# Optimization experiments

Hardware: AMD Instinct MI355X
Metric: run time of the kernel (lower is better)

## Reference

```python
import jax, jax.numpy as jnp
import numpy as np

H = 8192   # lattice vertex count (all levels, synthetic, == hash_cnt)
N0 = 8192  # output point count
F = 15     # permutohedral filter size: (t+1)^(d+1) - t^(d+1), t=1, d=3
NEG = 0.1  # LeakyReLU negative slope

def lrelu(x):
    return jnp.where(x >= 0, x, NEG * x)

def conv1x1(x, w, b):
    # x (B,C,N), w (O,C), b (O,)
    return jnp.einsum('oc,bcn->bon', w, x) + b[None, :, None]

def splat(feat, bary, offset, num):
    # barycentric scatter of point features onto lattice: (B,C,N)->(B,C,num)
    w = feat[:, :, None, :] * bary[:, None, :, :]  # (B,C,4,N)
    def one(wb, ob):
        C = wb.shape[0]
        return jax.ops.segment_sum(wb.reshape(C, -1).T, ob.reshape(-1), num_segments=num).T
    return jax.vmap(one)(w, offset)

def gather(lat, idx):
    # lat (B,C,H), idx (B,K,N) -> (B,C,K,N)
    return jax.vmap(lambda f, i: f[:, i])(lat, idx)

def slice_lat(lat, bary, offset):
    # barycentric interpolation from lattice back to points: (B,C,N)
    return jnp.einsum('bcjn,bjn->bcn', gather(lat, offset), bary)

def blur_mlp(lat, nbrs, w0, b0, w1, b1):
    # BilateralConvFlex blur: gather F lattice neighbors, 1x1-conv MLP (last_relu=False)
    g = gather(lat, nbrs)  # (B,C,F,H)
    B, C, Fk, Hk = g.shape
    h = lrelu(conv1x1(g.reshape(B, C * Fk, Hk), w0, b0))
    return conv1x1(h, w1, b1)

def corr_block(feat1_pts, feat2_lat, prev_pts, bary1, off1, out_bary, out_off,
               idx1, idx2, wc0, bc0, wc1, bc1, wo0, bo0, wo1, bo1):
    # BilateralCorrelationFlex: splat pc1, hash-indexed patch correlation with pc2
    # lattice, per-displacement corr MLP, flatten over displacements, out MLP, slice.
    L1 = splat(feat1_pts, bary1, off1, H)                  # (B,C,H)
    x = gather(L1, idx1) * gather(feat2_lat, idx2)         # (B,C,F,H)
    if prev_pts is not None:
        P1 = splat(prev_pts, bary1, off1, H)
        x = jnp.concatenate([x, gather(P1, idx1)], axis=1)
    h = lrelu(jnp.einsum('oc,bcfh->bofh', wc0, x) + bc0[None, :, None, None])
    h = lrelu(jnp.einsum('oc,bcfh->bofh', wc1, h) + bc1[None, :, None, None])
    B, Co, Fk, Hk = h.shape
    h = lrelu(conv1x1(h.reshape(B, Co * Fk, Hk), wo0, bo0))
    h = conv1x1(h, wo1, bo1)                               # last_relu=False
    return slice_lat(h, out_bary, out_off)

def setup_inputs():
    key = jax.random.key(0)
    ks = iter(jax.random.split(key, 100))
    def randn(shape):
        return jax.random.normal(next(ks), shape, dtype=jnp.float32)
    def bary(n):
        b = jax.random.uniform(next(ks), (1, 4, n), dtype=jnp.float32)
        return b / jnp.sum(b, axis=1, keepdims=True)
    def ridx(shape, hi):
        return jax.random.randint(next(ks), shape, 0, hi)
    def W(o, c):
        return jax.random.normal(next(ks), (o, c), dtype=jnp.float32) / np.float32(np.sqrt(c))
    def bias(o):
        return jax.random.normal(next(ks), (o,), dtype=jnp.float32) * 0.01
    inp = {}
    for n in ['feat0_1', 'feat0_2', 'feat0_4', 'feat1_1', 'feat1_2', 'feat1_4']:
        inp[n] = randn((1, 32, H))
    for n in ['g2_pc1_el_minus_gr', 'g2_pc2_el_minus_gr', 'g1_pc1_el_minus_gr', 'g1_pc2_el_minus_gr']:
        inp[n] = randn((1, 4, H))
    inp['g2_pc1_barycentric'] = bary(H); inp['g2_pc2_barycentric'] = bary(H)
    inp['g1_pc1_barycentric'] = bary(H); inp['g1_pc2_barycentric'] = bary(H)
    inp['g0_pc1_barycentric'] = bary(N0)
    for n in ['g2_pc1_lattice_offset', 'g2_pc2_lattice_offset', 'g1_pc1_lattice_offset', 'g1_pc2_lattice_offset']:
        inp[n] = ridx((1, 4, H), H)
    inp['g0_pc1_lattice_offset'] = ridx((1, 4, N0), H)
    for n in ['g1_pc1_blur_neighbors', 'g1_pc2_blur_neighbors', 'g0_pc1_blur_neighbors', 'g0_pc2_blur_neighbors',
              'g1_pc1_corr_indices', 'g1_pc2_corr_indices', 'g0_pc1_corr_indices', 'g0_pc2_corr_indices']:
        inp[n] = ridx((1, F, H), H)
    inp['w_embed2'] = W(128, 32); inp['b_embed2'] = bias(128)
    inp['w_embed1'] = W(256, 32); inp['b_embed1'] = bias(256)
    inp['w_up2_0'] = W(256, 132 * F); inp['b_up2_0'] = bias(256)
    inp['w_up2_1'] = W(256, 256); inp['b_up2_1'] = bias(256)
    inp['w_up1_0'] = W(512, 516 * F); inp['b_up1_0'] = bias(512)
    inp['w_up1_1'] = W(512, 512); inp['b_up1_1'] = bias(512)
    inp['w_c2_corr0'] = W(32, 256); inp['b_c2_corr0'] = bias(32)
    inp['w_c2_corr1'] = W(32, 32); inp['b_c2_corr1'] = bias(32)
    inp['w_c2_out0'] = W(256, 32 * F); inp['b_c2_out0'] = bias(256)
    inp['w_c2_out1'] = W(256, 256); inp['b_c2_out1'] = bias(256)
    inp['w_c1_corr0'] = W(32, 512 + 256); inp['b_c1_corr0'] = bias(32)
    inp['w_c1_corr1'] = W(32, 32); inp['b_c1_corr1'] = bias(32)
    inp['w_c1_out0'] = W(512, 32 * F); inp['b_c1_out0'] = bias(512)
    inp['w_c1_out1'] = W(512, 512); inp['b_c1_out1'] = bias(512)
    inp['w_s4'] = W(512, 512); inp['b_s4'] = bias(512)
    inp['w_s2'] = W(256, 512); inp['b_s2'] = bias(256)
    inp['w_s1'] = W(3, 256); inp['b_s1'] = bias(3)
    return inp

def reference(feat0_1, feat0_2, feat0_4, feat1_1, feat1_2, feat1_4,
              g2_pc1_el_minus_gr, g2_pc2_el_minus_gr, g1_pc1_el_minus_gr, g1_pc2_el_minus_gr,
              g2_pc1_barycentric, g2_pc2_barycentric, g1_pc1_barycentric, g1_pc2_barycentric, g0_pc1_barycentric,
              g2_pc1_lattice_offset, g2_pc2_lattice_offset, g1_pc1_lattice_offset, g1_pc2_lattice_offset, g0_pc1_lattice_offset,
              g1_pc1_blur_neighbors, g1_pc2_blur_neighbors, g0_pc1_blur_neighbors, g0_pc2_blur_neighbors,
              g1_pc1_corr_indices, g1_pc2_corr_indices, g0_pc1_corr_indices, g0_pc2_corr_indices,
              w_embed2, b_embed2, w_embed1, b_embed1,
              w_up2_0, b_up2_0, w_up2_1, b_up2_1, w_up1_0, b_up1_0, w_up1_1, b_up1_1,
              w_c2_corr0, b_c2_corr0, w_c2_corr1, b_c2_corr1, w_c2_out0, b_c2_out0, w_c2_out1, b_c2_out1,
              w_c1_corr0, b_c1_corr0, w_c1_corr1, b_c1_corr1, w_c1_out0, b_c1_out0, w_c1_out1, b_c1_out1,
              w_s4, b_s4, w_s2, b_s2, w_s1, b_s1):
    # conv4_embed and feat*_4 are defined but unused in the original forward.
    f0_2 = lrelu(conv1x1(feat0_2, w_embed2, b_embed2))
    f1_2 = lrelu(conv1x1(feat1_2, w_embed2, b_embed2))
    blur0 = blur_mlp(jnp.concatenate([g2_pc1_el_minus_gr, f0_2], axis=1),
                     g1_pc1_blur_neighbors, w_up2_0, b_up2_0, w_up2_1, b_up2_1)
    pcl0_2 = slice_lat(blur0, g2_pc1_barycentric, g2_pc1_lattice_offset)
    pcl0_2_to_1 = slice_lat(blur0, g1_pc1_barycentric, g1_pc1_lattice_offset)
    blur1 = blur_mlp(jnp.concatenate([g2_pc2_el_minus_gr, f1_2], axis=1),
                     g1_pc2_blur_neighbors, w_up2_0, b_up2_0, w_up2_1, b_up2_1)
    pcl1_2 = slice_lat(blur1, g2_pc2_barycentric, g2_pc2_lattice_offset)
    pcl1_2_to_1 = slice_lat(blur1, g1_pc2_barycentric, g1_pc2_lattice_offset)
    corr2 = corr_block(pcl0_2, pcl1_2, None, g2_pc1_barycentric, g2_pc1_lattice_offset,
                       g1_pc1_barycentric, g1_pc1_lattice_offset,
                       g1_pc1_corr_indices, g1_pc2_corr_indices,
                       w_c2_corr0, b_c2_corr0, w_c2_corr1, b_c2_corr1,
                       w_c2_out0, b_c2_out0, w_c2_out1, b_c2_out1)
    f0_1 = lrelu(conv1x1(feat0_1, w_embed1, b_embed1))
    f1_1 = lrelu(conv1x1(feat1_1, w_embed1, b_embed1))
    lat0 = blur_mlp(jnp.concatenate([g1_pc1_el_minus_gr, pcl0_2_to_1, f0_1], axis=1),
                    g0_pc1_blur_neighbors, w_up1_0, b_up1_0, w_up1_1, b_up1_1)
    pcl0_1 = slice_lat(lat0, g1_pc1_barycentric, g1_pc1_lattice_offset)
    lat1 = blur_mlp(jnp.concatenate([g1_pc2_el_minus_gr, pcl1_2_to_1, f1_1], axis=1),
                    g0_pc2_blur_neighbors, w_up1_0, b_up1_0, w_up1_1, b_up1_1)
    pcl1_1 = slice_lat(lat1, g1_pc2_barycentric, g1_pc2_lattice_offset)
    corr1 = corr_block(pcl0_1, pcl1_1, corr2, g1_pc1_barycentric, g1_pc1_lattice_offset,
                       g0_pc1_barycentric, g0_pc1_lattice_offset,
                       g0_pc1_corr_indices, g0_pc2_corr_indices,
                       w_c1_corr0, b_c1_corr0, w_c1_corr1, b_c1_corr1,
                       w_c1_out0, b_c1_out0, w_c1_out1, b_c1_out1)
    res = lrelu(conv1x1(corr1, w_s4, b_s4))
    res = lrelu(conv1x1(res, w_s2, b_s2))
    return conv1x1(res, w_s1, b_s1)  # (1, 3, N0)
```

## Files before the change

kernel.cpp:

```cpp
#include <hip/hip_runtime.h>
#include <hip/hip_bf16.h>

#define HDIM 8192
#define FK 15

typedef __attribute__((ext_vector_type(8))) short bf16x8;
typedef __attribute__((ext_vector_type(4))) float f32x4;

__device__ __forceinline__ void gload_lds16(const void* g, void* l) {
    __builtin_amdgcn_global_load_lds(
        (const __attribute__((address_space(1))) void*)g,
        (__attribute__((address_space(3))) void*)l, 16, 0, 0);
}

__global__ void k_pack(const float* __restrict__ W, __hip_bfloat16* __restrict__ P,
                       int O, int C, int Cp, int Fk, int mode) {
    int e = blockIdx.x * 256 + threadIdx.x;
    int total = Fk * Cp * O;
    if (e >= total) return;
    int j = e & 7;
    int lane = (e >> 3) & 63;
    int tile = e >> 9;
    int OT = O >> 4;
    int ot = tile % OT, kt = tile / OT;
    int o = ot * 16 + (lane & 15);
    int kk = kt * 32 + (lane >> 4) * 8 + j;
    float v;
    if (mode == 1) {
        int f = kk / Cp, c = kk % Cp;
        v = (c < C) ? W[(size_t)o * C * Fk + (size_t)c * Fk + f] : 0.f;
    } else if (mode == 2) {
        int f = kk >> 5, oo = kk & 31;
        v = W[(size_t)o * 480 + oo * 15 + f];
    } else {
        v = W[(size_t)o * C + kk];
    }
    P[e] = __float2bfloat16(v);
}

__global__ void k_copy_el(const float* __restrict__ el, __hip_bfloat16* __restrict__ catT,
                          int N, int ld) {
    int n = blockIdx.x * 256 + threadIdx.x;
    if (n >= N) return;
#pragma unroll
    for (int j = 0; j < 4; ++j)
        catT[(size_t)n * ld + j] = __float2bfloat16(el[(size_t)j * N + n]);
}

__global__ __launch_bounds__(256) void k_embed(const float* __restrict__ X,
                                               const float* __restrict__ W,
                                               const float* __restrict__ b,
                                               __hip_bfloat16* __restrict__ outT,
                                               int N, int O, int ld, int coff) {
    __shared__ float Xs[32][65];
    int tid = threadIdx.x;
    int n0 = blockIdx.x * 64;
    for (int e = tid; e < 32 * 64; e += 256) {
        int nn = e & 63, c = e >> 6;
        Xs[c][nn] = X[(size_t)c * N + n0 + nn];
    }
    __syncthreads();
    int ol = tid & 63, nl = tid >> 6;
    for (int o0 = 0; o0 < O; o0 += 64) {
        int o = o0 + ol;
        float wv[32];
#pragma unroll
        for (int c = 0; c < 32; ++c) wv[c] = W[o * 32 + c];
        float bv = b[o];
        for (int nn = nl; nn < 64; nn += 4) {
            float acc = bv;
#pragma unroll
            for (int c = 0; c < 32; ++c) acc += wv[c] * Xs[c][nn];
            acc = acc >= 0.f ? acc : 0.1f * acc;
            outT[(size_t)(n0 + nn) * ld + coff + o] = __float2bfloat16(acc);
        }
    }
}

struct W4 { bf16x8 r0, r1, r2, r3; };

template<int OG, int HG, int MR>
__global__ __launch_bounds__(512, 2) void k_blur_fat(
    const __hip_bfloat16* __restrict__ A0b, const __hip_bfloat16* __restrict__ A1b,
    const int* __restrict__ n0, const int* __restrict__ n1,
    const __hip_bfloat16* __restrict__ Wb, float* __restrict__ hbuf,
    int Cp, int O, int H) {
    __shared__ short abuf[3 * 4096];
    __shared__ int idx_s[8 * 128];
    int z = blockIdx.z;
    int strm = z >> 1, kh = z & 1;
    const unsigned short* A = (const unsigned short*)(strm ? A1b : A0b);
    const int* nbrs = strm ? n1 : n0;
    int CpT = Cp >> 5, OT = O >> 4;
    int fbeg = kh ? 8 : 0;
    int fcnt = kh ? (FK - 8) : 8;
    int S = fcnt * CpT;
    float* outp = hbuf + (size_t)z * ((size_t)H * (size_t)O);
    const unsigned short* Wp = (const unsigned short*)Wb;
    int tid = threadIdx.x, lane = tid & 63, wid = tid >> 6;
    int r16 = lane & 15, g = lane >> 4;
    int og = (OG == 8) ? wid : (wid & 3);
    int hg = (OG == 8) ? 0 : (wid >> 2);
    int h0 = blockIdx.x * 128;
    int srow = tid >> 2;
    int sgseg = (tid & 3) ^ ((tid >> 3) & 3);
    int pseg = g ^ ((r16 >> 1) & 3);
    int hgbase = hg * (MR * 16);
    char* abase = (char*)abuf;

    for (int e = tid; e < fcnt * 128; e += 512)
        idx_s[e] = nbrs[(size_t)(fbeg + (e >> 7)) * H + h0 + (e & 127)];
    __syncthreads();

    f32x4 acc[MR][4];
#pragma unroll
    for (int m = 0; m < MR; ++m)
#pragma unroll
        for (int n = 0; n < 4; ++n) acc[m][n] = (f32x4){0.f, 0.f, 0.f, 0.f};

    W4 wA, wB, wC;
    int tS = 0, cS = 0, fS = 0;

#define STAGE_AW(SLOTA, W)                                                         \
    do {                                                                           \
        int gi = idx_s[fS * 128 + srow];                                           \
        gload_lds16(A + (size_t)gi * Cp + cS * 32 + sgseg * 8,                     \
                    abase + (SLOTA) * 8192 + wid * 1024);                          \
        const unsigned short* wbp =                                                \
            Wp + ((size_t)(((fbeg + fS) * CpT + cS) * OT + og * 4)) * 512 + lane * 8; \
        W.r0 = *(const bf16x8*)(wbp);                                              \
        W.r1 = *(const bf16x8*)(wbp + 512);                                        \
        W.r2 = *(const bf16x8*)(wbp + 1024);                                       \
        W.r3 = *(const bf16x8*)(wbp + 1536);                                       \
        if (tS < S - 1) { ++tS; if (++cS == CpT) { cS = 0; ++fS; } }               \
    } while (0)

#define FITER(SLOT, WCUR, WNXT)                                                    \
    do {                                                                           \
        __builtin_amdgcn_sched_barrier(0);                                         \
        asm volatile("s_waitcnt vmcnt(5)" ::: "memory");                           \
        __builtin_amdgcn_sched_barrier(0);                                         \
        __builtin_amdgcn_s_barrier();                                              \
        __builtin_amdgcn_sched_barrier(0);                                         \
        STAGE_AW(((SLOT) + 2) % 3, WNXT);                                          \
        const short* ab = abuf + (SLOT) * 4096;                                    \
        bf16x8 av[MR];                                                             \
        _Pragma("unroll")                                                          \
        for (int rb = 0; rb < MR; ++rb)                                            \
            av[rb] = *(const bf16x8*)(ab + (hgbase + rb * 16 + r16) * 32 + pseg * 8); \
        _Pragma("unroll")                                                          \
        for (int rb = 0; rb < MR; ++rb) {                                          \
            acc[rb][0] = __builtin_amdgcn_mfma_f32_16x16x32_bf16(av[rb], WCUR.r0, acc[rb][0], 0, 0, 0); \
            acc[rb][1] = __builtin_amdgcn_mfma_f32_16x16x32_bf16(av[rb], WCUR.r1, acc[rb][1], 0, 0, 0); \
            acc[rb][2] = __builtin_amdgcn_mfma_f32_16x16x32_bf16(av[rb], WCUR.r2, acc[rb][2], 0, 0, 0); \
            acc[rb][3] = __builtin_amdgcn_mfma_f32_16x16x32_bf16(av[rb], WCUR.r3, acc[rb][3], 0, 0, 0); \
        }                                                                          \
    } while (0)

    STAGE_AW(0, wA);
    STAGE_AW(1, wB);
    for (int t = 0; t < S; t += 3) {
        FITER(0, wA, wC);
        if (t + 1 < S) FITER(1, wB, wA);
        if (t + 2 < S) FITER(2, wC, wB);
    }
#undef FITER
#undef STAGE_AW

#pragma unroll
    for (int n = 0; n < 4; ++n) {
        int o = og * 64 + n * 16 + r16;
#pragma unroll
        for (int m = 0; m < MR; ++m)
#pragma unroll
            for (int i = 0; i < 4; ++i)
                outp[(size_t)(h0 + hgbase + m * 16 + g * 4 + i) * O + o] = acc[m][n][i];
    }
}

__global__ void k_comb(const float* __restrict__ p, const float* __restrict__ bias,
                       __hip_bfloat16* __restrict__ out, int NO, int Om) {
    int i = blockIdx.x * 256 + threadIdx.x;
    int stride = gridDim.x * 256;
    for (; i < NO; i += stride) {
        float v = p[i] + p[i + NO] + bias[i & Om];
        v = v >= 0.f ? v : 0.1f * v;
        out[i] = __float2bfloat16(v);
    }
}

#define DEF_PIPE_VARS                                                              \
    bf16x8 a00, a01, w00, w01, w02, w03;                                           \
    bf16x8 a10, a11, w10, w11, w12, w13;                                           \
    bf16x8 a20, a21, w20, w21, w22, w23;

#define LOADST(J, TEND, FEND)                                                      \
    do {                                                                           \
        const unsigned short* a0p = A + (size_t)i0c * Cp + cL * 32 + g * 8;        \
        const unsigned short* a1p = A + (size_t)i1c * Cp + cL * 32 + g * 8;        \
        a##J##0 = *(const bf16x8*)a0p;                                             \
        a##J##1 = *(const bf16x8*)a1p;                                             \
        const unsigned short* wbp = Wp + ((size_t)(tL * OT + otb)) * 512 + lane * 8; \
        w##J##0 = *(const bf16x8*)(wbp);                                           \
        w##J##1 = *(const bf16x8*)(wbp + 512);                                     \
        w##J##2 = *(const bf16x8*)(wbp + 1024);                                    \
        w##J##3 = *(const bf16x8*)(wbp + 1536);                                    \
        if (tL < (TEND) - 1) {                                                     \
            ++tL;                                                                  \
            if (++cL == CpT) {                                                     \
                cL = 0; ++fL;                                                      \
                i0c = i0n; i1c = i1n;                                              \
                if (fL + 1 < (FEND)) {                                             \
                    i0n = nbrs ? nbrs[(size_t)(fL + 1) * H + hrow] : hrow;         \
                    i1n = nbrs ? nbrs[(size_t)(fL + 1) * H + hrow + 16] : (hrow + 16); \
                }                                                                  \
            }                                                                      \
        }                                                                          \
    } while (0)

#define MFMAST(J)                                                                  \
// ... 91 lines not shown
}

__global__ void k_slice_b(const float* __restrict__ latT, const float* __restrict__ bary,
                          const int* __restrict__ off, __hip_bfloat16* __restrict__ outT,
                          int N, int C, int ld, int coff) {
    int cl = threadIdx.x & 63, rr = threadIdx.x >> 6;
    int n = blockIdx.x * 4 + rr;
    int c = blockIdx.y * 64 + cl;
    float s = 0.f;
#pragma unroll
    for (int j = 0; j < 4; ++j) {
        int o = off[(size_t)j * N + n];
        float w = bary[(size_t)j * N + n];
        s += latT[(size_t)o * C + c] * w;
    }
    outT[(size_t)n * ld + coff + c] = __float2bfloat16(s);
}

__global__ void k_splat(const float* __restrict__ featT, const float* __restrict__ bary,
                        const int* __restrict__ off, float* __restrict__ latT,
                        int N, int C) {
    int cl = threadIdx.x & 63, rr = threadIdx.x >> 6;
    int n = blockIdx.x * 4 + rr;
    int c = blockIdx.y * 64 + cl;
    float v = featT[(size_t)n * C + c];
#pragma unroll
    for (int j = 0; j < 4; ++j) {
        int o = off[(size_t)j * N + n];
        float w = bary[(size_t)j * N + n];
        atomicAdd(&latT[(size_t)o * C + c], v * w);
    }
}

__global__ __launch_bounds__(256) void k_corr_mfma(const float* __restrict__ L1T,
                                                   const float* __restrict__ f2T,
                                                   const float* __restrict__ P1T,
                                                   const int* __restrict__ idx1,
                                                   const int* __restrict__ idx2,
                                                   const __hip_bfloat16* __restrict__ W0p,
                                                   const float* __restrict__ b0,
                                                   const __hip_bfloat16* __restrict__ W1p,
                                                   const float* __restrict__ b1,
                                                   __hip_bfloat16* __restrict__ h1T,
                                                   int H, int C1, int C2) {
    __shared__ __hip_bfloat16 As[64 * 72];
    __shared__ __hip_bfloat16 A0s[64 * 40];
    __shared__ int i1s[64], i2s[64];
    int tid = threadIdx.x;
    int p0 = blockIdx.x * 64;
    int f = p0 >> 13;
    int h0 = p0 & (HDIM - 1);
    if (tid < 64) {
        i1s[tid] = idx1[(size_t)f * H + h0 + tid];
        i2s[tid] = idx2[(size_t)f * H + h0 + tid];
    }
    __syncthreads();
    int lane = tid & 63, wid = tid >> 6;
    int wh = wid * 16;
    int r16 = lane & 15, g = lane >> 4;
    int srow = tid >> 2, sseg = tid & 3;
    int K = C1 + C2;
    const unsigned short* W0u = (const unsigned short*)W0p;
    const unsigned short* W1u = (const unsigned short*)W1p;
    f32x4 acc[2];
    acc[0] = (f32x4){0.f, 0.f, 0.f, 0.f};
    acc[1] = (f32x4){0.f, 0.f, 0.f, 0.f};

    for (int c0 = 0; c0 < K; c0 += 64) {
        int cb = c0 + sseg * 16;
        float x[16];
        if (cb < C1) {
            const float4* a4 = (const float4*)(L1T + (size_t)i1s[srow] * C1 + cb);
            const float4* b4 = (const float4*)(f2T + (size_t)i2s[srow] * C1 + cb);
#pragma unroll
            for (int q = 0; q < 4; ++q) {
                float4 av = a4[q], bv = b4[q];
                x[q * 4 + 0] = av.x * bv.x; x[q * 4 + 1] = av.y * bv.y;
                x[q * 4 + 2] = av.z * bv.z; x[q * 4 + 3] = av.w * bv.w;
            }
        } else {
            const float4* a4 = (const float4*)(P1T + (size_t)i1s[srow] * C2 + (cb - C1));
#pragma unroll
            for (int q = 0; q < 4; ++q) {
                float4 av = a4[q];
                x[q * 4 + 0] = av.x; x[q * 4 + 1] = av.y;
                x[q * 4 + 2] = av.z; x[q * 4 + 3] = av.w;
            }
        }
        __syncthreads();
        __hip_bfloat16* dst = &As[srow * 72 + sseg * 16];
#pragma unroll
        for (int q = 0; q < 16; ++q) dst[q] = __float2bfloat16(x[q]);
        __syncthreads();
        int ktg = c0 >> 5;
#pragma unroll
        for (int kt = 0; kt < 2; ++kt) {
            bf16x8 a = *(const bf16x8*)(&As[(wh + r16) * 72 + kt * 32 + g * 8]);
            const unsigned short* wb = W0u + (size_t)((ktg + kt) * 2) * 512 + lane * 8;
            bf16x8 bf0 = *(const bf16x8*)(wb);
            bf16x8 bf1 = *(const bf16x8*)(wb + 512);
            acc[0] = __builtin_amdgcn_mfma_f32_16x16x32_bf16(a, bf0, acc[0], 0, 0, 0);
            acc[1] = __builtin_amdgcn_mfma_f32_16x16x32_bf16(a, bf1, acc[1], 0, 0, 0);
        }
    }
    __syncthreads();
#pragma unroll
    for (int ot = 0; ot < 2; ++ot) {
        int o = ot * 16 + r16;
        float bv = b0[o];
#pragma unroll
        for (int i = 0; i < 4; ++i) {
            int pr = wh + g * 4 + i;
            float v = acc[ot][i] + bv;
            v = v >= 0.f ? v : 0.1f * v;
            A0s[pr * 40 + o] = __float2bfloat16(v);
        }
    }
    __syncthreads();
    bf16x8 a1 = *(const bf16x8*)(&A0s[(wh + r16) * 40 + g * 8]);
// ... 49 lines not shown

    char* base = (char*)d_ws;
    size_t off = 0;
    auto allocB = [&](size_t elems) -> __hip_bfloat16* {
        __hip_bfloat16* r = (__hip_bfloat16*)(base + off);
        off += ((elems * 2 + 255) / 256) * 256;
        return r;
    };
    auto allocF = [&](size_t elems) -> float* {
        float* r = (float*)(base + off);
        off += ((elems * 4 + 255) / 256) * 256;
        return r;
    };

    __hip_bfloat16* pw_up2   = allocB((size_t)15 * 160 * 256);
    __hip_bfloat16* pw_up1   = allocB((size_t)15 * 544 * 512);
    __hip_bfloat16* pw_up2_1 = allocB((size_t)256 * 256);
    __hip_bfloat16* pw_up1_1 = allocB((size_t)512 * 512);
    __hip_bfloat16* pw_c2o   = allocB((size_t)480 * 256);
    __hip_bfloat16* pw_c2o1  = allocB((size_t)256 * 256);
    __hip_bfloat16* pw_c1o   = allocB((size_t)480 * 512);
    __hip_bfloat16* pw_c1o1  = allocB((size_t)512 * 512);
    __hip_bfloat16* pw_s4    = allocB((size_t)512 * 512);
    __hip_bfloat16* pw_s2    = allocB((size_t)512 * 256);
    __hip_bfloat16* pw_cc20  = allocB((size_t)256 * 32);
    __hip_bfloat16* pw_cc21  = allocB((size_t)32 * 32);
    __hip_bfloat16* pw_cc10  = allocB((size_t)768 * 32);
    __hip_bfloat16* pw_cc11  = allocB((size_t)32 * 32);
    __hip_bfloat16* catb2a = allocB((size_t)N * 160);
    __hip_bfloat16* catb2b = allocB((size_t)N * 160);
    __hip_bfloat16* catb1a = allocB((size_t)N * 544);
    __hip_bfloat16* catb1b = allocB((size_t)N * 544);
    __hip_bfloat16* ab512a = allocB((size_t)N * 512);
    __hip_bfloat16* ab512b = allocB((size_t)N * 512);
    __hip_bfloat16* ab256a = allocB((size_t)N * 256);
    __hip_bfloat16* ab256b = allocB((size_t)N * 256);
    __hip_bfloat16* h1b    = allocB((size_t)N * 480);
    __hip_bfloat16* corr1b = allocB((size_t)N * 512);
    float* T512a  = allocF((size_t)N * 512);
    float* T512b  = allocF((size_t)N * 512);
    float* pcl512 = allocF((size_t)N * 512);
    float* pcl01  = allocF((size_t)N * 512);
    float* pcl11  = allocF((size_t)N * 512);
    float* SL256  = allocF((size_t)N * 256);
    float* corr2T = allocF((size_t)N * 256);
    float* hbuf   = allocF((size_t)4 * N * 512);
    float* pclA = pcl512;
    float* pclB = pcl512 + (size_t)N * 256;
    float* SL512 = pcl512;
    float* SP256 = SL256;
    (void)ws_size; (void)in_sizes; (void)n_in; (void)out_size;

    auto pack = [&](const float* W, __hip_bfloat16* P, int O, int C, int Cp, int Fk, int mode) {
        int total = Fk * Cp * O;
        k_pack<<<(total + 255) / 256, 256, 0, stream>>>(W, P, O, C, Cp, Fk, mode);
    };
    pack(F32(32), pw_up2,   256, 132, 160, 15, 1);
    pack(F32(36), pw_up1,   512, 516, 544, 15, 1);
    pack(F32(34), pw_up2_1, 256, 256, 256, 1, 0);
    pack(F32(38), pw_up1_1, 512, 512, 512, 1, 0);
    pack(F32(44), pw_c2o,   256, 480, 480, 1, 2);
    pack(F32(46), pw_c2o1,  256, 256, 256, 1, 0);
    pack(F32(52), pw_c1o,   512, 480, 480, 1, 2);
    pack(F32(54), pw_c1o1,  512, 512, 512, 1, 0);
    pack(F32(56), pw_s4,    512, 512, 512, 1, 0);
    pack(F32(58), pw_s2,    256, 512, 512, 1, 0);
    pack(F32(40), pw_cc20,  32, 256, 256, 1, 0);
    pack(F32(42), pw_cc21,  32, 32, 32, 1, 0);
    pack(F32(48), pw_cc10,  32, 768, 768, 1, 0);
    pack(F32(50), pw_cc11,  32, 32, 32, 1, 0);

    hipMemsetAsync(catb2a, 0, (size_t)N * 160 * 2, stream);
    hipMemsetAsync(catb2b, 0, (size_t)N * 160 * 2, stream);
    hipMemsetAsync(catb1a, 0, (size_t)N * 544 * 2, stream);
    hipMemsetAsync(catb1b, 0, (size_t)N * 544 * 2, stream);
    hipMemsetAsync(SL256,  0, (size_t)N * 256 * 4, stream);

    k_copy_el<<<32, 256, 0, stream>>>(F32(6), catb2a, N, 160);
    k_embed<<<128, 256, 0, stream>>>(F32(1), F32(28), F32(29), catb2a, N, 128, 160, 4);
    k_copy_el<<<32, 256, 0, stream>>>(F32(7), catb2b, N, 160);
    k_embed<<<128, 256, 0, stream>>>(F32(4), F32(28), F32(29), catb2b, N, 128, 160, 4);
    k_blur_fat<4, 2, 4><<<dim3(64, 1, 4), 512, 0, stream>>>(catb2a, catb2b, I32(20), I32(21),
                                                            pw_up2, hbuf, 160, 256, N);
    k_comb<<<2048, 256, 0, stream>>>(hbuf, F32(33), ab256a, N * 256, 255);
    k_comb<<<2048, 256, 0, stream>>>(hbuf + (size_t)2 * N * 256, F32(33), ab256b, N * 256, 255);
    k_mfma_gemm<<<dim3(64, 4, 2), 256, 0, stream>>>(ab256a, nullptr, pw_up2_1, F32(35),
                                                    T512a, nullptr, 256, 1, 256, N, 0,
                                                    ab256b, T512b, nullptr);
    k_slice<<<dim3(2048, 4), 256, 0, stream>>>(T512a, F32(10), I32(15), pclA, N, 256, 256, 0);
    k_slice_b<<<dim3(2048, 4), 256, 0, stream>>>(T512a, F32(12), I32(17), catb1a, N, 256, 544, 4);
    k_slice<<<dim3(2048, 4), 256, 0, stream>>>(T512b, F32(11), I32(16), pclB, N, 256, 256, 0);
    k_slice_b<<<dim3(2048, 4), 256, 0, stream>>>(T512b, F32(13), I32(18), catb1b, N, 256, 544, 4);

    k_splat<<<dim3(2048, 4), 256, 0, stream>>>(pclA, F32(10), I32(15), SL256, N, 256);
    k_corr_mfma<<<FK * HDIM / 64, 256, 0, stream>>>(SL256, pclB, (const float*)nullptr,
                                                    I32(24), I32(25), pw_cc20, F32(41),
                                                    pw_cc21, F32(43), h1b, N, 256, 0);
    k_mfma_gemm<<<dim3(64, 4), 256, 0, stream>>>(h1b, nullptr, pw_c2o, F32(45),
                                                 nullptr, ab256a, 480, 1, 256, N, 1,
                                                 nullptr, nullptr, nullptr);
    k_mfma_gemm<<<dim3(64, 4), 256, 0, stream>>>(ab256a, nullptr, pw_c2o1, F32(47),
                                                 T512a, nullptr, 256, 1, 256, N, 0,
                                                 nullptr, nullptr, nullptr);
    k_slice<<<dim3(2048, 4), 256, 0, stream>>>(T512a, F32(12), I32(17), corr2T, N, 256, 256, 0);

    k_copy_el<<<32, 256, 0, stream>>>(F32(8), catb1a, N, 544);
    k_embed<<<128, 256, 0, stream>>>(F32(0), F32(30), F32(31), catb1a, N, 256, 544, 260);
    k_copy_el<<<32, 256, 0, stream>>>(F32(9), catb1b, N, 544);
    k_embed<<<128, 256, 0, stream>>>(F32(3), F32(30), F32(31), catb1b, N, 256, 544, 260);
    k_blur_fat<8, 1, 8><<<dim3(64, 1, 4), 512, 0, stream>>>(catb1a, catb1b, I32(22), I32(23),
                                                            pw_up1, hbuf, 544, 512, N);
    k_comb<<<2048, 256, 0, stream>>>(hbuf, F32(37), ab512a, N * 512, 511);
    k_comb<<<2048, 256, 0, stream>>>(hbuf + (size_t)2 * N * 512, F32(37), ab512b, N * 512, 511);
    k_mfma_gemm<<<dim3(64, 8, 2), 256, 0, stream>>>(ab512a, nullptr, pw_up1_1, F32(39),
                                                    T512a, nullptr, 512, 1, 512, N, 0,
                                                    ab512b, T512b, nullptr);
    k_slice<<<dim3(2048, 8), 256, 0, stream>>>(T512a, F32(12), I32(17), pcl01, N, 512, 512, 0);
    k_slice<<<dim3(2048, 8), 256, 0, stream>>>(T512b, F32(13), I32(18), pcl11, N, 512, 512, 0);

    hipMemsetAsync(SL512, 0, (size_t)N * 512 * 4, stream);
    k_splat<<<dim3(2048, 8), 256, 0, stream>>>(pcl01, F32(12), I32(17), SL512, N, 512);
    hipMemsetAsync(SP256, 0, (size_t)N * 256 * 4, stream);
    k_splat<<<dim3(2048, 4), 256, 0, stream>>>(corr2T, F32(12), I32(17), SP256, N, 256);
    k_corr_mfma<<<FK * HDIM / 64, 256, 0, stream>>>(SL512, pcl11, SP256,
                                                    I32(26), I32(27), pw_cc10, F32(49),
                                                    pw_cc11, F32(51), h1b, N, 512, 256);
    k_mfma_gemm<<<dim3(64, 8), 256, 0, stream>>>(h1b, nullptr, pw_c1o, F32(53),
                                                 nullptr, ab512a, 480, 1, 512, N, 1,
                                                 nullptr, nullptr, nullptr);
    k_mfma_gemm<<<dim3(64, 8), 256, 0, stream>>>(ab512a, nullptr, pw_c1o1, F32(55),
                                                 T512a, nullptr, 512, 1, 512, N, 0,
                                                 nullptr, nullptr, nullptr);
    k_slice_b<<<dim3(2048, 8), 256, 0, stream>>>(T512a, F32(14), I32(19), corr1b, N, 512, 512, 0);

    k_mfma_gemm<<<dim3(64, 8), 256, 0, stream>>>(corr1b, nullptr, pw_s4, F32(57),
                                                 nullptr, ab512a, 512, 1, 512, N, 1,
                                                 nullptr, nullptr, nullptr);
    k_mfma_gemm<<<dim3(64, 4), 256, 0, stream>>>(ab512a, nullptr, pw_s2, F32(59),
                                                 T512a, nullptr, 512, 1, 256, N, 1,
                                                 nullptr, nullptr, nullptr);
    k_final<<<32, 256, 0, stream>>>(T512a, F32(60), F32(61), (float*)d_out, N);
}
```

Before: 818.5 us.

## Fuse split-K partial-sum combine into blur second GEMM; convert splatted lattices to bf16

Replaces the k_comb passes and the separate bf16 GEMM with a new k_gemm_ps kernel. It reads the two fp32 split-K partial sums directly, adds the bias, applies LeakyReLU, converts to bf16 in registers and feeds the MFMAs, so the intermediate bf16 activation buffers are never written or re-read. It also adds k_cvt passes that turn the splatted fp32 lattices into bf16 before the correlation kernel, which halves the bytes of the randomly indexed gathers there (15 gathers per lattice row). The cost is extra conversion launches, a GEMM that loads fp32 A operands without LDS staging, and slightly lower precision for the lattice values.

```diff
diff --git a/kernel.cpp b/kernel.cpp
--- a/kernel.cpp
+++ b/kernel.cpp
@@ -5,12 +5,20 @@
 #define FK 15
 
 typedef __attribute__((ext_vector_type(8))) short bf16x8;
+typedef __attribute__((ext_vector_type(8))) unsigned short u16x8;
 typedef __attribute__((ext_vector_type(4))) float f32x4;
 
 __device__ __forceinline__ void gload_lds16(const void* g, void* l) {
     __builtin_amdgcn_global_load_lds(
         (const __attribute__((address_space(1))) void*)g,
         (__attribute__((address_space(3))) void*)l, 16, 0, 0);
+}
+
+__device__ __forceinline__ float b2f(unsigned short s) {
+    unsigned u = (unsigned)s << 16;
+    float f;
+    __builtin_memcpy(&f, &u, 4);
+    return f;
 }
 
 __global__ void k_pack(const float* __restrict__ W, __hip_bfloat16* __restrict__ P,
@@ -75,6 +83,16 @@
             outT[(size_t)(n0 + nn) * ld + coff + o] = __float2bfloat16(acc);
         }
     }
+}
+
+__global__ void k_cvt(const float* __restrict__ in, __hip_bfloat16* __restrict__ out, int n) {
+    int i = (blockIdx.x * 256 + threadIdx.x) * 4;
+    if (i >= n) return;
+    float4 v = *(const float4*)(in + i);
+    out[i + 0] = __float2bfloat16(v.x);
+    out[i + 1] = __float2bfloat16(v.y);
+    out[i + 2] = __float2bfloat16(v.z);
+    out[i + 3] = __float2bfloat16(v.w);
 }
 
 struct W4 { bf16x8 r0, r1, r2, r3; };
@@ -178,14 +196,108 @@
     }
 }
 
-__global__ void k_comb(const float* __restrict__ p, const float* __restrict__ bias,
-                       __hip_bfloat16* __restrict__ out, int NO, int Om) {
-    int i = blockIdx.x * 256 + threadIdx.x;
-    int stride = gridDim.x * 256;
-    for (; i < NO; i += stride) {
-        float v = p[i] + p[i + NO] + bias[i & Om];
-        v = v >= 0.f ? v : 0.1f * v;
-        out[i] = __float2bfloat16(v);
+__global__ __launch_bounds__(256) void k_gemm_ps(const float* __restrict__ ps,
+                                                 const float* __restrict__ abias,
+                                                 const __hip_bfloat16* __restrict__ Wb,
+                                                 const float* __restrict__ bias,
+                                                 float* __restrict__ outF0,
+                                                 float* __restrict__ outF1,
+                                                 int Cp, int O, int H, int act) {
+    size_t NO = (size_t)H * Cp;
+    const float* PS = ps + (size_t)blockIdx.z * 2 * NO;
+    float* outF = blockIdx.z ? outF1 : outF0;
+    const unsigned short* Wp = (const unsigned short*)Wb;
+    int tid = threadIdx.x, lane = tid & 63, w = tid >> 6;
+    int r16 = lane & 15, g = lane >> 4;
+    int h0 = blockIdx.x * 128, o0 = blockIdx.y * 64;
+    int OT = O >> 4, S = Cp >> 5;
+    int otb = o0 >> 4;
+    int w32 = w * 32;
+    int hrow = h0 + w32 + r16;
+
+    f32x4 acc[2][4];
+#pragma unroll
+    for (int m = 0; m < 2; ++m)
+#pragma unroll
+        for (int n = 0; n < 4; ++n) acc[m][n] = (f32x4){0.f, 0.f, 0.f, 0.f};
+
+    float4 pA00, pA01, pA02, pA03, pB00, pB01, pB02, pB03, bb00, bb01;
+    float4 pA10, pA11, pA12, pA13, pB10, pB11, pB12, pB13, bb10, bb11;
+    float4 pA20, pA21, pA22, pA23, pB20, pB21, pB22, pB23, bb20, bb21;
+    bf16x8 w00, w01, w02, w03, w10, w11, w12, w13, w20, w21, w22, w23;
+    int cL = 0;
+
+#define PSLD(J)                                                                    \
+    do {                                                                           \
+        const float* p0_ = PS + (size_t)hrow * Cp + cL * 32 + g * 8;               \
+        const float* p1_ = p0_ + 16 * Cp;                                          \
+        pA##J##0 = *(const float4*)(p0_);      pA##J##1 = *(const float4*)(p0_ + 4); \
+        pA##J##2 = *(const float4*)(p0_ + NO); pA##J##3 = *(const float4*)(p0_ + NO + 4); \
+        pB##J##0 = *(const float4*)(p1_);      pB##J##1 = *(const float4*)(p1_ + 4); \
+        pB##J##2 = *(const float4*)(p1_ + NO); pB##J##3 = *(const float4*)(p1_ + NO + 4); \
+        bb##J##0 = *(const float4*)(abias + cL * 32 + g * 8);                      \
+        bb##J##1 = *(const float4*)(abias + cL * 32 + g * 8 + 4);                  \
+        const unsigned short* wbp_ = Wp + ((size_t)(cL * OT + otb)) * 512 + lane * 8; \
+        w##J##0 = *(const bf16x8*)(wbp_);        w##J##1 = *(const bf16x8*)(wbp_ + 512); \
+        w##J##2 = *(const bf16x8*)(wbp_ + 1024); w##J##3 = *(const bf16x8*)(wbp_ + 1536); \
+        if (cL < S - 1) ++cL;                                                      \
+    } while (0)
+
+#define PSMM(J)                                                                    \
+    do {                                                                           \
+        bf16x8 a0_, a1_;                                                           \
+        _Pragma("unroll")                                                          \
+        for (int k_ = 0; k_ < 4; ++k_) {                                           \
+            float e0 = pA##J##0[k_] + pA##J##2[k_] + bb##J##0[k_];                 \
+            e0 = e0 >= 0.f ? e0 : 0.1f * e0;                                       \
+            ((__hip_bfloat16*)&a0_)[k_] = __float2bfloat16(e0);                    \
+            float e1 = pA##J##1[k_] + pA##J##3[k_] + bb##J##1[k_];                 \
+            e1 = e1 >= 0.f ? e1 : 0.1f * e1;                                       \
+            ((__hip_bfloat16*)&a0_)[4 + k_] = __float2bfloat16(e1);                \
+            float f0 = pB##J##0[k_] + pB##J##2[k_] + bb##J##0[k_];                 \
+            f0 = f0 >= 0.f ? f0 : 0.1f * f0;                                       \
+            ((__hip_bfloat16*)&a1_)[k_] = __float2bfloat16(f0);                    \
+            float f1 = pB##J##1[k_] + pB##J##3[k_] + bb##J##1[k_];                 \
+            f1 = f1 >= 0.f ? f1 : 0.1f * f1;                                       \
+            ((__hip_bfloat16*)&a1_)[4 + k_] = __float2bfloat16(f1);                \
+        }                                                                          \
+        acc[0][0] = __builtin_amdgcn_mfma_f32_16x16x32_bf16(a0_, w##J##0, acc[0][0], 0, 0, 0); \
+        acc[0][1] = __builtin_amdgcn_mfma_f32_16x16x32_bf16(a0_, w##J##1, acc[0][1], 0, 0, 0); \
+        acc[0][2] = __builtin_amdgcn_mfma_f32_16x16x32_bf16(a0_, w##J##2, acc[0][2], 0, 0, 0); \
+        acc[0][3] = __builtin_amdgcn_mfma_f32_16x16x32_bf16(a0_, w##J##3, acc[0][3], 0, 0, 0); \
+        acc[1][0] = __builtin_amdgcn_mfma_f32_16x16x32_bf16(a1_, w##J##0, acc[1][0], 0, 0, 0); \
+        acc[1][1] = __builtin_amdgcn_mfma_f32_16x16x32_bf16(a1_, w##J##1, acc[1][1], 0, 0, 0); \
+        acc[1][2] = __builtin_amdgcn_mfma_f32_16x16x32_bf16(a1_, w##J##2, acc[1][2], 0, 0, 0); \
+        acc[1][3] = __builtin_amdgcn_mfma_f32_16x16x32_bf16(a1_, w##J##3, acc[1][3], 0, 0, 0); \
+    } while (0)
+
+    PSLD(0);
+    PSLD(1);
+    for (int sb = 0; sb < S; sb += 3) {
+        PSLD(2);
+        PSMM(0);
+        PSLD(0);
+        if (sb + 1 < S) PSMM(1);
+        PSLD(1);
+        if (sb + 2 < S) PSMM(2);
+    }
+#undef PSLD
+#undef PSMM
+
+#pragma unroll
+    for (int n = 0; n < 4; ++n) {
+        int o = o0 + n * 16 + r16;
+        float bv = bias[o];
+#pragma unroll
+        for (int m = 0; m < 2; ++m) {
+#pragma unroll
+            for (int i = 0; i < 4; ++i) {
+                int h = h0 + w32 + m * 16 + g * 4 + i;
+                float v = acc[m][n][i] + bv;
+                if (act) v = v >= 0.f ? v : 0.1f * v;
+                outF[(size_t)h * O + o] = v;
+            }
+        }
     }
 }
 
@@ -343,9 +455,9 @@
     }
 }
 
-__global__ __launch_bounds__(256) void k_corr_mfma(const float* __restrict__ L1T,
+__global__ __launch_bounds__(256) void k_corr_mfma(const __hip_bfloat16* __restrict__ L1b,
                                                    const float* __restrict__ f2T,
-                                                   const float* __restrict__ P1T,
+                                                   const __hip_bfloat16* __restrict__ P1b,
                                                    const int* __restrict__ idx1,
                                                    const int* __restrict__ idx2,
                                                    const __hip_bfloat16* __restrict__ W0p,
@@ -357,6 +469,8 @@
     __shared__ __hip_bfloat16 As[64 * 72];
     __shared__ __hip_bfloat16 A0s[64 * 40];
     __shared__ int i1s[64], i2s[64];
+    const unsigned short* L1u = (const unsigned short*)L1b;
+    const unsigned short* P1u = (const unsigned short*)P1b;
     int tid = threadIdx.x;
     int p0 = blockIdx.x * 64;
     int f = p0 >> 13;
@@ -381,21 +495,24 @@
         int cb = c0 + sseg * 16;
         float x[16];
         if (cb < C1) {
-            const float4* a4 = (const float4*)(L1T + (size_t)i1s[srow] * C1 + cb);
+            u16x8 av0 = *(const u16x8*)(L1u + (size_t)i1s[srow] * C1 + cb);
+            u16x8 av1 = *(const u16x8*)(L1u + (size_t)i1s[srow] * C1 + cb + 8);
             const float4* b4 = (const float4*)(f2T + (size_t)i2s[srow] * C1 + cb);
-#pragma unroll
-            for (int q = 0; q < 4; ++q) {
-                float4 av = a4[q], bv = b4[q];
-                x[q * 4 + 0] = av.x * bv.x; x[q * 4 + 1] = av.y * bv.y;
-                x[q * 4 + 2] = av.z * bv.z; x[q * 4 + 3] = av.w * bv.w;
+            float4 bv0 = b4[0], bv1 = b4[1], bv2 = b4[2], bv3 = b4[3];
+#pragma unroll
+            for (int u = 0; u < 4; ++u) {
+                x[u]      = b2f(av0[u])     * bv0[u];
+                x[4 + u]  = b2f(av0[4 + u]) * bv1[u];
+                x[8 + u]  = b2f(av1[u])     * bv2[u];
+                x[12 + u] = b2f(av1[4 + u]) * bv3[u];
             }
         } else {
-            const float4* a4 = (const float4*)(P1T + (size_t)i1s[srow] * C2 + (cb - C1));
-#pragma unroll
-            for (int q = 0; q < 4; ++q) {
-                float4 av = a4[q];
-                x[q * 4 + 0] = av.x; x[q * 4 + 1] = av.y;
-                x[q * 4 + 2] = av.z; x[q * 4 + 3] = av.w;
+            u16x8 p0v = *(const u16x8*)(P1u + (size_t)i1s[srow] * C2 + (cb - C1));
+            u16x8 p1v = *(const u16x8*)(P1u + (size_t)i1s[srow] * C2 + (cb - C1) + 8);
+#pragma unroll
+            for (int u = 0; u < 8; ++u) {
+                x[u] = b2f(p0v[u]);
+                x[8 + u] = b2f(p1v[u]);
             }
         }
         __syncthreads();
@@ -511,11 +628,12 @@
     __hip_bfloat16* catb1a = allocB((size_t)N * 544);
     __hip_bfloat16* catb1b = allocB((size_t)N * 544);
     __hip_bfloat16* ab512a = allocB((size_t)N * 512);
-    __hip_bfloat16* ab512b = allocB((size_t)N * 512);
     __hip_bfloat16* ab256a = allocB((size_t)N * 256);
-    __hip_bfloat16* ab256b = allocB((size_t)N * 256);
     __hip_bfloat16* h1b    = allocB((size_t)N * 480);
     __hip_bfloat16* corr1b = allocB((size_t)N * 512);
+    __hip_bfloat16* SL256b = allocB((size_t)N * 256);
+    __hip_bfloat16* SL512b = allocB((size_t)N * 512);
+    __hip_bfloat16* SP256b = allocB((size_t)N * 256);
     float* T512a  = allocF((size_t)N * 512);
     float* T512b  = allocF((size_t)N * 512);
     float* pcl512 = allocF((size_t)N * 512);
@@ -561,18 +679,16 @@
     k_embed<<<128, 256, 0, stream>>>(F32(4), F32(28), F32(29), catb2b, N, 128, 160, 4);
     k_blur_fat<4, 2, 4><<<dim3(64, 1, 4), 512, 0, stream>>>(catb2a, catb2b, I32(20), I32(21),
                                                             pw_up2, hbuf, 160, 256, N);
-    k_comb<<<2048, 256, 0, stream>>>(hbuf, F32(33), ab256a, N * 256, 255);
-    k_comb<<<2048, 256, 0, stream>>>(hbuf + (size_t)2 * N * 256, F32(33), ab256b, N * 256, 255);
-    k_mfma_gemm<<<dim3(64, 4, 2), 256, 0, stream>>>(ab256a, nullptr, pw_up2_1, F32(35),
-                                                    T512a, nullptr, 256, 1, 256, N, 0,
-                                                    ab256b, T512b, nullptr);
+    k_gemm_ps<<<dim3(64, 4, 2), 256, 0, stream>>>(hbuf, F32(33), pw_up2_1, F32(35),
+                                                  T512a, T512b, 256, 256, N, 0);
     k_slice<<<dim3(2048, 4), 256, 0, stream>>>(T512a, F32(10), I32(15), pclA, N, 256, 256, 0);
     k_slice_b<<<dim3(2048, 4), 256, 0, stream>>>(T512a, F32(12), I32(17), catb1a, N, 256, 544, 4);
     k_slice<<<dim3(2048, 4), 256, 0, stream>>>(T512b, F32(11), I32(16), pclB, N, 256, 256, 0);
     k_slice_b<<<dim3(2048, 4), 256, 0, stream>>>(T512b, F32(13), I32(18), catb1b, N, 256, 544, 4);
 
     k_splat<<<dim3(2048, 4), 256, 0, stream>>>(pclA, F32(10), I32(15), SL256, N, 256);
-    k_corr_mfma<<<FK * HDIM / 64, 256, 0, stream>>>(SL256, pclB, (const float*)nullptr,
+    k_cvt<<<(N * 256 / 4 + 255) / 256, 256, 0, stream>>>(SL256, SL256b, N * 256);
+    k_corr_mfma<<<FK * HDIM / 64, 256, 0, stream>>>(SL256b, pclB, (const __hip_bfloat16*)nullptr,
                                                     I32(24), I32(25), pw_cc20, F32(41),
                                                     pw_cc21, F32(43), h1b, N, 256, 0);
     k_mfma_gemm<<<dim3(64, 4), 256, 0, stream>>>(h1b, nullptr, pw_c2o, F32(45),
@@ -589,11 +705,8 @@
     k_embed<<<128, 256, 0, stream>>>(F32(3), F32(30), F32(31), catb1b, N, 256, 544, 260);
     k_blur_fat<8, 1, 8><<<dim3(64, 1, 4), 512, 0, stream>>>(catb1a, catb1b, I32(22), I32(23),
                                                             pw_up1, hbuf, 544, 512, N);
-    k_comb<<<2048, 256, 0, stream>>>(hbuf, F32(37), ab512a, N * 512, 511);
-    k_comb<<<2048, 256, 0, stream>>>(hbuf + (size_t)2 * N * 512, F32(37), ab512b, N * 512, 511);
-    k_mfma_gemm<<<dim3(64, 8, 2), 256, 0, stream>>>(ab512a, nullptr, pw_up1_1, F32(39),
-                                                    T512a, nullptr, 512, 1, 512, N, 0,
-                                                    ab512b, T512b, nullptr);
+    k_gemm_ps<<<dim3(64, 8, 2), 256, 0, stream>>>(hbuf, F32(37), pw_up1_1, F32(39),
+                                                  T512a, T512b, 512, 512, N, 0);
     k_slice<<<dim3(2048, 8), 256, 0, stream>>>(T512a, F32(12), I32(17), pcl01, N, 512, 512, 0);
     k_slice<<<dim3(2048, 8), 256, 0, stream>>>(T512b, F32(13), I32(18), pcl11, N, 512, 512, 0);
 
@@ -601,7 +714,9 @@
     k_splat<<<dim3(2048, 8), 256, 0, stream>>>(pcl01, F32(12), I32(17), SL512, N, 512);
     hipMemsetAsync(SP256, 0, (size_t)N * 256 * 4, stream);
     k_splat<<<dim3(2048, 4), 256, 0, stream>>>(corr2T, F32(12), I32(17), SP256, N, 256);
-    k_corr_mfma<<<FK * HDIM / 64, 256, 0, stream>>>(SL512, pcl11, SP256,
+    k_cvt<<<(N * 512 / 4 + 255) / 256, 256, 0, stream>>>(SL512, SL512b, N * 512);
+    k_cvt<<<(N * 256 / 4 + 255) / 256, 256, 0, stream>>>(SP256, SP256b, N * 256);
+    k_corr_mfma<<<FK * HDIM / 64, 256, 0, stream>>>(SL512b, pcl11, SP256b,
                                                     I32(26), I32(27), pw_cc10, F32(49),
                                                     pw_cc11, F32(51), h1b, N, 512, 256);
     k_mfma_gemm<<<dim3(64, 8), 256, 0, stream>>>(h1b, nullptr, pw_c1o, F32(53),
```

Result: no change. 830.1 us (+1.4%).

## Fuse blur split-K reduction into epilogue and feed bf16 lattices to corr

Applied to the files above, without the earlier changes.

The blur kernel no longer splits the filter taps across two blocks that write fp32 partials for a separate combine kernel. Each block now processes all taps for 64 lattice rows and applies bias and LeakyReLU before storing bf16 directly. Splatted lattices are converted to bf16 before the correlation kernel so its gathers read half the bytes. This adds small conversion kernels and a little rounding of the splat values, and halves per-block rows in blur, which may reduce weight reuse.

```diff
diff --git a/kernel.cpp b/kernel.cpp
--- a/kernel.cpp
+++ b/kernel.cpp
@@ -5,12 +5,20 @@
 #define FK 15
 
 typedef __attribute__((ext_vector_type(8))) short bf16x8;
+typedef __attribute__((ext_vector_type(8))) unsigned short u16x8;
 typedef __attribute__((ext_vector_type(4))) float f32x4;
 
 __device__ __forceinline__ void gload_lds16(const void* g, void* l) {
     __builtin_amdgcn_global_load_lds(
         (const __attribute__((address_space(1))) void*)g,
         (__attribute__((address_space(3))) void*)l, 16, 0, 0);
+}
+
+__device__ __forceinline__ float b2f(unsigned short s) {
+    unsigned u = (unsigned)s << 16;
+    float f;
+    __builtin_memcpy(&f, &u, 4);
+    return f;
 }
 
 __global__ void k_pack(const float* __restrict__ W, __hip_bfloat16* __restrict__ P,
@@ -77,39 +85,47 @@
     }
 }
 
+__global__ void k_cvt(const float* __restrict__ in, __hip_bfloat16* __restrict__ out, int n) {
+    int i = (blockIdx.x * 256 + threadIdx.x) * 4;
+    if (i >= n) return;
+    float4 v = *(const float4*)(in + i);
+    out[i + 0] = __float2bfloat16(v.x);
+    out[i + 1] = __float2bfloat16(v.y);
+    out[i + 2] = __float2bfloat16(v.z);
+    out[i + 3] = __float2bfloat16(v.w);
+}
+
 struct W4 { bf16x8 r0, r1, r2, r3; };
 
 template<int OG, int HG, int MR>
-__global__ __launch_bounds__(512, 2) void k_blur_fat(
+__global__ __launch_bounds__(512, 2) void k_blur_v2(
     const __hip_bfloat16* __restrict__ A0b, const __hip_bfloat16* __restrict__ A1b,
     const int* __restrict__ n0, const int* __restrict__ n1,
-    const __hip_bfloat16* __restrict__ Wb, float* __restrict__ hbuf,
+    const __hip_bfloat16* __restrict__ Wb, const float* __restrict__ bias,
+    __hip_bfloat16* __restrict__ out0, __hip_bfloat16* __restrict__ out1,
     int Cp, int O, int H) {
-    __shared__ short abuf[3 * 4096];
-    __shared__ int idx_s[8 * 128];
+    __shared__ short abuf[3 * 2048];
+    __shared__ int idx_s[FK * 64];
     int z = blockIdx.z;
-    int strm = z >> 1, kh = z & 1;
-    const unsigned short* A = (const unsigned short*)(strm ? A1b : A0b);
-    const int* nbrs = strm ? n1 : n0;
+    const unsigned short* A = (const unsigned short*)(z ? A1b : A0b);
+    const int* nbrs = z ? n1 : n0;
+    __hip_bfloat16* outB = z ? out1 : out0;
     int CpT = Cp >> 5, OT = O >> 4;
-    int fbeg = kh ? 8 : 0;
-    int fcnt = kh ? (FK - 8) : 8;
-    int S = fcnt * CpT;
-    float* outp = hbuf + (size_t)z * ((size_t)H * (size_t)O);
+    int S = FK * CpT;
     const unsigned short* Wp = (const unsigned short*)Wb;
     int tid = threadIdx.x, lane = tid & 63, wid = tid >> 6;
     int r16 = lane & 15, g = lane >> 4;
     int og = (OG == 8) ? wid : (wid & 3);
     int hg = (OG == 8) ? 0 : (wid >> 2);
-    int h0 = blockIdx.x * 128;
+    int h0 = blockIdx.x * 64;
     int srow = tid >> 2;
     int sgseg = (tid & 3) ^ ((tid >> 3) & 3);
     int pseg = g ^ ((r16 >> 1) & 3);
     int hgbase = hg * (MR * 16);
     char* abase = (char*)abuf;
 
-    for (int e = tid; e < fcnt * 128; e += 512)
-        idx_s[e] = nbrs[(size_t)(fbeg + (e >> 7)) * H + h0 + (e & 127)];
+    for (int e = tid; e < FK * 64; e += 512)
+        idx_s[e] = nbrs[(size_t)(e >> 6) * H + h0 + (e & 63)];
     __syncthreads();
 
     f32x4 acc[MR][4];
@@ -123,11 +139,13 @@
 
 #define STAGE_AW(SLOTA, W)                                                         \
     do {                                                                           \
-        int gi = idx_s[fS * 128 + srow];                                           \
-        gload_lds16(A + (size_t)gi * Cp + cS * 32 + sgseg * 8,                     \
-                    abase + (SLOTA) * 8192 + wid * 1024);                          \
+        if (wid < 4) {                                                             \
+            int gi = idx_s[fS * 64 + srow];                                        \
+            gload_lds16(A + (size_t)gi * Cp + cS * 32 + sgseg * 8,                 \
+                        abase + (SLOTA) * 4096 + wid * 1024);                      \
+        }                                                                          \
         const unsigned short* wbp =                                                \
-            Wp + ((size_t)(((fbeg + fS) * CpT + cS) * OT + og * 4)) * 512 + lane * 8; \
+            Wp + ((size_t)((fS * CpT + cS) * OT + og * 4)) * 512 + lane * 8;       \
         W.r0 = *(const bf16x8*)(wbp);                                              \
         W.r1 = *(const bf16x8*)(wbp + 512);                                        \
         W.r2 = *(const bf16x8*)(wbp + 1024);                                       \
@@ -143,7 +161,7 @@
         __builtin_amdgcn_s_barrier();                                              \
         __builtin_amdgcn_sched_barrier(0);                                         \
         STAGE_AW(((SLOT) + 2) % 3, WNXT);                                          \
-        const short* ab = abuf + (SLOT) * 4096;                                    \
+        const short* ab = abuf + (SLOT) * 2048;                                    \
         bf16x8 av[MR];                                                             \
         _Pragma("unroll")                                                          \
         for (int rb = 0; rb < MR; ++rb)                                            \
@@ -161,8 +179,8 @@
     STAGE_AW(1, wB);
     for (int t = 0; t < S; t += 3) {
         FITER(0, wA, wC);
-        if (t + 1 < S) FITER(1, wB, wA);
-        if (t + 2 < S) FITER(2, wC, wB);
+        FITER(1, wB, wA);
+        FITER(2, wC, wB);
     }
 #undef FITER
 #undef STAGE_AW
@@ -170,22 +188,16 @@
 #pragma unroll
     for (int n = 0; n < 4; ++n) {
         int o = og * 64 + n * 16 + r16;
+        float bv = bias[o];
 #pragma unroll
         for (int m = 0; m < MR; ++m)
 #pragma unroll
-            for (int i = 0; i < 4; ++i)
-                outp[(size_t)(h0 + hgbase + m * 16 + g * 4 + i) * O + o] = acc[m][n][i];
-    }
-}
-
-__global__ void k_comb(const float* __restrict__ p, const float* __restrict__ bias,
-                       __hip_bfloat16* __restrict__ out, int NO, int Om) {
-    int i = blockIdx.x * 256 + threadIdx.x;
-    int stride = gridDim.x * 256;
-    for (; i < NO; i += stride) {
-        float v = p[i] + p[i + NO] + bias[i & Om];
-        v = v >= 0.f ? v : 0.1f * v;
-        out[i] = __float2bfloat16(v);
+            for (int i = 0; i < 4; ++i) {
+                int h = h0 + hgbase + m * 16 + g * 4 + i;
+                float v = acc[m][n][i] + bv;
+                v = v >= 0.f ? v : 0.1f * v;
+                outB[(size_t)h * O + o] = __float2bfloat16(v);
+            }
     }
 }
 
@@ -343,9 +355,9 @@
     }
 }
 
-__global__ __launch_bounds__(256) void k_corr_mfma(const float* __restrict__ L1T,
+__global__ __launch_bounds__(256) void k_corr_mfma(const __hip_bfloat16* __restrict__ L1b,
                                                    const float* __restrict__ f2T,
-                                                   const float* __restrict__ P1T,
+                                                   const __hip_bfloat16* __restrict__ P1b,
                                                    const int* __restrict__ idx1,
                                                    const int* __restrict__ idx2,
                                                    const __hip_bfloat16* __restrict__ W0p,
@@ -357,6 +369,8 @@
     __shared__ __hip_bfloat16 As[64 * 72];
     __shared__ __hip_bfloat16 A0s[64 * 40];
     __shared__ int i1s[64], i2s[64];
+    const unsigned short* L1u = (const unsigned short*)L1b;
+    const unsigned short* P1u = (const unsigned short*)P1b;
     int tid = threadIdx.x;
     int p0 = blockIdx.x * 64;
     int f = p0 >> 13;
@@ -381,21 +395,24 @@
         int cb = c0 + sseg * 16;
         float x[16];
         if (cb < C1) {
-            const float4* a4 = (const float4*)(L1T + (size_t)i1s[srow] * C1 + cb);
+            u16x8 av0 = *(const u16x8*)(L1u + (size_t)i1s[srow] * C1 + cb);
+            u16x8 av1 = *(const u16x8*)(L1u + (size_t)i1s[srow] * C1 + cb + 8);
             const float4* b4 = (const float4*)(f2T + (size_t)i2s[srow] * C1 + cb);
-#pragma unroll
-            for (int q = 0; q < 4; ++q) {
-                float4 av = a4[q], bv = b4[q];
-                x[q * 4 + 0] = av.x * bv.x; x[q * 4 + 1] = av.y * bv.y;
-                x[q * 4 + 2] = av.z * bv.z; x[q * 4 + 3] = av.w * bv.w;
+            float4 bv0 = b4[0], bv1 = b4[1], bv2 = b4[2], bv3 = b4[3];
+#pragma unroll
+            for (int u = 0; u < 4; ++u) {
+                x[u]      = b2f(av0[u])     * bv0[u];
+                x[4 + u]  = b2f(av0[4 + u]) * bv1[u];
+                x[8 + u]  = b2f(av1[u])     * bv2[u];
+                x[12 + u] = b2f(av1[4 + u]) * bv3[u];
             }
         } else {
-            const float4* a4 = (const float4*)(P1T + (size_t)i1s[srow] * C2 + (cb - C1));
-#pragma unroll
-            for (int q = 0; q < 4; ++q) {
-                float4 av = a4[q];
-                x[q * 4 + 0] = av.x; x[q * 4 + 1] = av.y;
-                x[q * 4 + 2] = av.z; x[q * 4 + 3] = av.w;
+            u16x8 p0v = *(const u16x8*)(P1u + (size_t)i1s[srow] * C2 + (cb - C1));
+            u16x8 p1v = *(const u16x8*)(P1u + (size_t)i1s[srow] * C2 + (cb - C1) + 8);
+#pragma unroll
+            for (int u = 0; u < 8; ++u) {
+                x[u] = b2f(p0v[u]);
+                x[8 + u] = b2f(p1v[u]);
             }
         }
         __syncthreads();
@@ -516,6 +533,9 @@
     __hip_bfloat16* ab256b = allocB((size_t)N * 256);
     __hip_bfloat16* h1b    = allocB((size_t)N * 480);
     __hip_bfloat16* corr1b = allocB((size_t)N * 512);
+    __hip_bfloat16* SL256b = allocB((size_t)N * 256);
+    __hip_bfloat16* SL512b = allocB((size_t)N * 512);
+    __hip_bfloat16* SP256b = allocB((size_t)N * 256);
     float* T512a  = allocF((size_t)N * 512);
     float* T512b  = allocF((size_t)N * 512);
     float* pcl512 = allocF((size_t)N * 512);
@@ -523,7 +543,6 @@
     float* pcl11  = allocF((size_t)N * 512);
     float* SL256  = allocF((size_t)N * 256);
     float* corr2T = allocF((size_t)N * 256);
-    float* hbuf   = allocF((size_t)4 * N * 512);
     float* pclA = pcl512;
     float* pclB = pcl512 + (size_t)N * 256;
     float* SL512 = pcl512;
@@ -559,10 +578,9 @@
     k_embed<<<128, 256, 0, stream>>>(F32(1), F32(28), F32(29), catb2a, N, 128, 160, 4);
     k_copy_el<<<32, 256, 0, stream>>>(F32(7), catb2b, N, 160);
     k_embed<<<128, 256, 0, stream>>>(F32(4), F32(28), F32(29), catb2b, N, 128, 160, 4);
-    k_blur_fat<4, 2, 4><<<dim3(64, 1, 4), 512, 0, stream>>>(catb2a, catb2b, I32(20), I32(21),
-                                                            pw_up2, hbuf, 160, 256, N);
-    k_comb<<<2048, 256, 0, stream>>>(hbuf, F32(33), ab256a, N * 256, 255);
-    k_comb<<<2048, 256, 0, stream>>>(hbuf + (size_t)2 * N * 256, F32(33), ab256b, N * 256, 255);
+    k_blur_v2<4, 2, 2><<<dim3(128, 1, 2), 512, 0, stream>>>(catb2a, catb2b, I32(20), I32(21),
+                                                            pw_up2, F32(33), ab256a, ab256b,
+                                                            160, 256, N);
     k_mfma_gemm<<<dim3(64, 4, 2), 256, 0, stream>>>(ab256a, nullptr, pw_up2_1, F32(35),
                                                     T512a, nullptr, 256, 1, 256, N, 0,
                                                     ab256b, T512b, nullptr);
@@ -572,7 +590,8 @@
     k_slice_b<<<dim3(2048, 4), 256, 0, stream>>>(T512b, F32(13), I32(18), catb1b, N, 256, 544, 4);
 
     k_splat<<<dim3(2048, 4), 256, 0, stream>>>(pclA, F32(10), I32(15), SL256, N, 256);
-    k_corr_mfma<<<FK * HDIM / 64, 256, 0, stream>>>(SL256, pclB, (const float*)nullptr,
+    k_cvt<<<(N * 256 / 4 + 255) / 256, 256, 0, stream>>>(SL256, SL256b, N * 256);
+    k_corr_mfma<<<FK * HDIM / 64, 256, 0, stream>>>(SL256b, pclB, (const __hip_bfloat16*)nullptr,
                                                     I32(24), I32(25), pw_cc20, F32(41),
                                                     pw_cc21, F32(43), h1b, N, 256, 0);
     k_mfma_gemm<<<dim3(64, 4), 256, 0, stream>>>(h1b, nullptr, pw_c2o, F32(45),
@@ -587,10 +606,9 @@
     k_embed<<<128, 256, 0, stream>>>(F32(0), F32(30), F32(31), catb1a, N, 256, 544, 260);
     k_copy_el<<<32, 256, 0, stream>>>(F32(9), catb1b, N, 544);
     k_embed<<<128, 256, 0, stream>>>(F32(3), F32(30), F32(31), catb1b, N, 256, 544, 260);
-    k_blur_fat<8, 1, 8><<<dim3(64, 1, 4), 512, 0, stream>>>(catb1a, catb1b, I32(22), I32(23),
-                                                            pw_up1, hbuf, 544, 512, N);
-    k_comb<<<2048, 256, 0, stream>>>(hbuf, F32(37), ab512a, N * 512, 511);
-    k_comb<<<2048, 256, 0, stream>>>(hbuf + (size_t)2 * N * 512, F32(37), ab512b, N * 512, 511);
+    k_blur_v2<8, 1, 4><<<dim3(128, 1, 2), 512, 0, stream>>>(catb1a, catb1b, I32(22), I32(23),
+                                                            pw_up1, F32(37), ab512a, ab512b,
+                                                            544, 512, N);
     k_mfma_gemm<<<dim3(64, 8, 2), 256, 0, stream>>>(ab512a, nullptr, pw_up1_1, F32(39),
                                                     T512a, nullptr, 512, 1, 512, N, 0,
                                                     ab512b, T512b, nullptr);
@@ -601,7 +619,9 @@
     k_splat<<<dim3(2048, 8), 256, 0, stream>>>(pcl01, F32(12), I32(17), SL512, N, 512);
     hipMemsetAsync(SP256, 0, (size_t)N * 256 * 4, stream);
     k_splat<<<dim3(2048, 4), 256, 0, stream>>>(corr2T, F32(12), I32(17), SP256, N, 256);
-    k_corr_mfma<<<FK * HDIM / 64, 256, 0, stream>>>(SL512, pcl11, SP256,
+    k_cvt<<<(N * 512 / 4 + 255) / 256, 256, 0, stream>>>(SL512, SL512b, N * 512);
+    k_cvt<<<(N * 256 / 4 + 255) / 256, 256, 0, stream>>>(SP256, SP256b, N * 256);
+    k_corr_mfma<<<FK * HDIM / 64, 256, 0, stream>>>(SL512b, pcl11, SP256b,
                                                     I32(26), I32(27), pw_cc10, F32(49),
                                                     pw_cc11, F32(51), h1b, N, 512, 256);
     k_mfma_gemm<<<dim3(64, 8), 256, 0, stream>>>(h1b, nullptr, pw_c1o, F32(53),
```

Measured after the change: 806.4 us. About the same (-1.5%).
